# Kernel optimization log

Measured on AMD Instinct MI355X. Metric: run time of the kernel, lower is better.

## Reference

```python
import jax, jax.numpy as jnp
import numpy as np

B, T, DQ, DV, UNITS = 32, 2048, 1024, 1024, 1024


def setup_inputs() -> dict:
    key = jax.random.key(0)
    ks = jax.random.split(key, 11)
    s_q = 1.0 / np.sqrt(DQ)
    s_v = 1.0 / np.sqrt(DV)
    s_u = 1.0 / np.sqrt(UNITS)
    return {
        "query": jax.random.normal(ks[0], (B, DQ), jnp.float32),
        "values": jax.random.normal(ks[1], (B, T, DV), jnp.float32),
        "prev_coverage": jax.random.uniform(ks[2], (B, T, 1), jnp.float32),
        "Wh": jax.random.normal(ks[3], (DQ, UNITS), jnp.float32) * s_q,
        "bh": jnp.zeros((UNITS,), jnp.float32),
        "Ws": jax.random.normal(ks[4], (DV, UNITS), jnp.float32) * s_v,
        "bs": jnp.zeros((UNITS,), jnp.float32),
        "Wc": jax.random.normal(ks[5], (1, UNITS), jnp.float32),
        "bc": jnp.zeros((UNITS,), jnp.float32),
        "Vw": jax.random.normal(ks[6], (UNITS, 1), jnp.float32) * s_u,
        "Vb": jnp.zeros((1,), jnp.float32),
    }


def reference(query, values, prev_coverage, Wh, bh, Ws, bs, Wc, bc, Vw, Vb):
    # query: [B, DQ] -> [B, 1, UNITS] (broadcast over time)
    q_proj = (query @ Wh + bh)[:, None, :]
    # values: [B, T, DV] -> [B, T, UNITS]
    v_proj = jnp.einsum('btd,du->btu', values, Ws) + bs
    # prev_coverage: [B, T, 1] -> [B, T, UNITS]
    c_proj = prev_coverage * Wc[0] + bc
    # score: [B, T, 1] via inline MLP
    score = jnp.tanh(q_proj + v_proj + c_proj) @ Vw + Vb
    # softmax over time axis (axis=1)
    attention_weights = jax.nn.softmax(score, axis=1)  # [B, T, 1]
    coverage = attention_weights + prev_coverage       # [B, T, 1]
    context_vector = jnp.sum(attention_weights * values, axis=1)  # [B, DV]
    return context_vector, jnp.squeeze(attention_weights, -1), coverage
```

## Files before the change

kernel.cpp:

```cpp
#include <hip/hip_runtime.h>
#include <hip/hip_bf16.h>
#include <stdint.h>

#define NB 32
#define NT 2048
#define ND 1024
#define NU 1024

typedef __attribute__((ext_vector_type(8))) short bf16x8;
typedef __attribute__((ext_vector_type(4))) float f32x4;
typedef __attribute__((ext_vector_type(4))) unsigned short us4;

__device__ __forceinline__ unsigned short f2bf(float f) {
  unsigned int u = __float_as_uint(f);
  u = (u + 0x7fffu + ((u >> 16) & 1u)) >> 16;
  return (unsigned short)u;
}

__device__ __forceinline__ float tanh_fast(float x) {
  x = fminf(10.0f, fmaxf(-10.0f, x));
  float t = __expf(2.0f * x);
  return 1.0f - 2.0f * __builtin_amdgcn_rcpf(t + 1.0f);
}

__global__ void wst_kernel(const float* __restrict__ Ws,
                           unsigned short* __restrict__ Wst) {
  __shared__ float tile[32][33];
  int d0 = blockIdx.x * 32, u0 = blockIdx.y * 32;
  int c = threadIdx.x & 31, r8 = threadIdx.x >> 5;
#pragma unroll
  for (int i = 0; i < 4; ++i) {
    int rr = i * 8 + r8;
    tile[rr][c] = Ws[(size_t)(d0 + rr) * NU + u0 + c];
  }
  __syncthreads();
#pragma unroll
  for (int i = 0; i < 4; ++i) {
    int rr = i * 8 + r8;
    Wst[(size_t)(u0 + rr) * ND + d0 + c] = f2bf(tile[c][rr]);
  }
}

__global__ void qb_kernel(const float* __restrict__ query,
                          const float* __restrict__ Wh,
                          const float* __restrict__ bh,
                          const float* __restrict__ bs,
                          const float* __restrict__ bc,
                          float* __restrict__ qb) {
  int b = blockIdx.x, tid = threadIdx.x;
  int u = tid * 4;
  float ax = bh[u + 0] + bs[u + 0] + bc[u + 0];
  float ay = bh[u + 1] + bs[u + 1] + bc[u + 1];
  float az = bh[u + 2] + bs[u + 2] + bc[u + 2];
  float aw = bh[u + 3] + bs[u + 3] + bc[u + 3];
  const float* q = query + (size_t)b * ND;
  const float4* W4 = (const float4*)Wh;
  for (int d = 0; d < ND; ++d) {
    float qv = q[d];
    float4 w = W4[d * 256 + tid];
    ax = fmaf(qv, w.x, ax);
    ay = fmaf(qv, w.y, ay);
    az = fmaf(qv, w.z, az);
    aw = fmaf(qv, w.w, aw);
  }
  float4 o; o.x = ax; o.y = ay; o.z = az; o.w = aw;
  ((float4*)(qb + (size_t)b * NU))[tid] = o;
}

__launch_bounds__(256)
__global__ void score_gemm(const float* __restrict__ values,
                           const unsigned short* __restrict__ Wst,
                           const float* __restrict__ qb,
                           const float* __restrict__ cov,
                           const float* __restrict__ Wc,
                           const float* __restrict__ Vw,
                           float* __restrict__ scores) {
  const int uc = blockIdx.x;
  const int tc = blockIdx.y;
  const int b  = blockIdx.z;
  const int t0 = tc * 128, u0 = uc * 128;
  const int tid = threadIdx.x;

  __shared__ unsigned short As[128 * 40];
  __shared__ unsigned short Bs[128 * 40];
  __shared__ float covs[128], qbs[128], wcs[128], vws[128];

  if (tid < 128) {
    covs[tid] = cov[(size_t)b * NT + t0 + tid];
    qbs[tid]  = qb[(size_t)b * NU + u0 + tid];
    wcs[tid]  = Wc[u0 + tid];
    vws[tid]  = Vw[u0 + tid];
  }

  f32x4 acc[4][4];
#pragma unroll
  for (int i = 0; i < 4; ++i)
#pragma unroll
    for (int j = 0; j < 4; ++j)
      acc[i][j] = (f32x4){0.f, 0.f, 0.f, 0.f};

  const int lane = tid & 63;
  const int wave = tid >> 6;
  const int wm = wave >> 1, wn = wave & 1;
  const int q = lane >> 4, ln = lane & 15;

  const int ar = tid >> 3;
  const int ac = (tid & 7) * 4;
  const int brow = tid >> 2;
  const int bcol = (tid & 3) * 8;

  const float* Abase = values + (size_t)(b * NT + t0) * ND;
  const unsigned short* Bbase = Wst + (size_t)u0 * ND;

  for (int kk = 0; kk < ND; kk += 32) {
#pragma unroll
    for (int p = 0; p < 4; ++p) {
      int row = p * 32 + ar;
      float4 v = *(const float4*)(Abase + (size_t)row * ND + kk + ac);
      us4 h;
      h.x = f2bf(v.x); h.y = f2bf(v.y); h.z = f2bf(v.z); h.w = f2bf(v.w);
      *(us4*)&As[row * 40 + ac] = h;
    }
#pragma unroll
    for (int p = 0; p < 2; ++p) {
      int row = p * 64 + brow;
      uint4 v = *(const uint4*)(Bbase + (size_t)row * ND + kk + bcol);
      *(uint4*)&Bs[row * 40 + bcol] = v;
    }
    __syncthreads();

    bf16x8 a[4], bb[4];
#pragma unroll
    for (int i = 0; i < 4; ++i) {
      a[i]  = *(const bf16x8*)&As[(wm * 64 + i * 16 + ln) * 40 + q * 8];
      bb[i] = *(const bf16x8*)&Bs[(wn * 64 + i * 16 + ln) * 40 + q * 8];
    }
#pragma unroll
    for (int i = 0; i < 4; ++i)
#pragma unroll
      for (int j = 0; j < 4; ++j)
        acc[i][j] = __builtin_amdgcn_mfma_f32_16x16x32_bf16(a[i], bb[j], acc[i][j], 0, 0, 0);
    __syncthreads();
  }

  float part[4][4];
#pragma unroll
  for (int tm = 0; tm < 4; ++tm)
#pragma unroll
    for (int r = 0; r < 4; ++r) part[tm][r] = 0.f;

#pragma unroll
  for (int tn = 0; tn < 4; ++tn) {
    int n = wn * 64 + tn * 16 + ln;
    float qv = qbs[n], wc = wcs[n], vw = vws[n];
#pragma unroll
    for (int tm = 0; tm < 4; ++tm) {
#pragma unroll
      for (int r = 0; r < 4; ++r) {
        int m = wm * 64 + tm * 16 + q * 4 + r;
        float pre = acc[tm][tn][r] + qv + covs[m] * wc;
        part[tm][r] += vw * tanh_fast(pre);
      }
    }
  }
#pragma unroll
  for (int tm = 0; tm < 4; ++tm) {
#pragma unroll
    for (int r = 0; r < 4; ++r) {
      float v = part[tm][r];
      v += __shfl_xor(v, 1);
      v += __shfl_xor(v, 2);
      v += __shfl_xor(v, 4);
      v += __shfl_xor(v, 8);
      if (ln == 0) {
        int m = wm * 64 + tm * 16 + q * 4 + r;
        atomicAdd(&scores[(size_t)b * NT + t0 + m], v);
      }
    }
  }
}

__global__ void softmax_stats(const float* __restrict__ scores,
                              float* __restrict__ stats) {
  int b = blockIdx.x, tid = threadIdx.x;
  __shared__ float red[4], red2[4];
  const float* s = scores + (size_t)b * NT;
  float m = -1e30f;
  for (int t = tid; t < NT; t += 256) m = fmaxf(m, s[t]);
#pragma unroll
  for (int off = 1; off < 64; off <<= 1) m = fmaxf(m, __shfl_xor(m, off));
  if ((tid & 63) == 0) red[tid >> 6] = m;
  __syncthreads();
  m = fmaxf(fmaxf(red[0], red[1]), fmaxf(red[2], red[3]));
  float l = 0.f;
  for (int t = tid; t < NT; t += 256) l += __expf(s[t] - m);
#pragma unroll
  for (int off = 1; off < 64; off <<= 1) l += __shfl_xor(l, off);
  if ((tid & 63) == 0) red2[tid >> 6] = l;
  __syncthreads();
  if (tid == 0) {
    l = red2[0] + red2[1] + red2[2] + red2[3];
    stats[b] = m;
    stats[32 + b] = 1.0f / l;
  }
}

__global__ void weights_kernel(const float* __restrict__ scores,
                               const float* __restrict__ stats,
                               const float* __restrict__ cov,
                               float* __restrict__ out) {
  int idx = blockIdx.x * 256 + threadIdx.x;
  int b = idx >> 11;
  float w = __expf(scores[idx] - stats[b]) * stats[32 + b];
  out[32768 + idx] = w;
  out[32768 + 65536 + idx] = w + cov[idx];
}

__global__ void context_kernel(const float* __restrict__ values,
                               const float* __restrict__ attn,
                               float* __restrict__ ctx) {
  int b = blockIdx.y, t0 = blockIdx.x * 128, tid = threadIdx.x;
  const float4* v4 = (const float4*)(values + (size_t)b * NT * ND);
  const float* w = attn + (size_t)b * NT + t0;
  float ax = 0.f, ay = 0.f, az = 0.f, aw = 0.f;
  for (int t = 0; t < 128; ++t) {
    float wt = w[t];
    float4 x = v4[(size_t)(t0 + t) * 256 + tid];
    ax = fmaf(wt, x.x, ax);
    ay = fmaf(wt, x.y, ay);
    az = fmaf(wt, x.z, az);
    aw = fmaf(wt, x.w, aw);
  }
  float* c = ctx + (size_t)b * ND + tid * 4;
  atomicAdd(c + 0, ax);
  atomicAdd(c + 1, ay);
  atomicAdd(c + 2, az);
  atomicAdd(c + 3, aw);
}

extern "C" void kernel_launch(void* const* d_in, const int* in_sizes, int n_in,
                              void* d_out, int out_size, void* d_ws, size_t ws_size,
                              hipStream_t stream) {
  (void)in_sizes; (void)n_in; (void)out_size; (void)ws_size;
  const float* query  = (const float*)d_in[0];
  const float* values = (const float*)d_in[1];
  const float* cov    = (const float*)d_in[2];
  const float* Wh     = (const float*)d_in[3];
  const float* bh     = (const float*)d_in[4];
  const float* Ws     = (const float*)d_in[5];
  const float* bs     = (const float*)d_in[6];
  const float* Wc     = (const float*)d_in[7];
  const float* bc     = (const float*)d_in[8];
  const float* Vw     = (const float*)d_in[9];

  char* ws = (char*)d_ws;
  unsigned short* Wst = (unsigned short*)ws;
  float* qb     = (float*)(ws + 2u * 1024 * 1024);
  float* scores = (float*)(ws + 2u * 1024 * 1024 + 128u * 1024);
  float* stats  = (float*)(ws + 2u * 1024 * 1024 + 384u * 1024);

  float* out = (float*)d_out;

  hipMemsetAsync(scores, 0, (size_t)NB * NT * sizeof(float), stream);
  hipMemsetAsync(out, 0, (size_t)NB * ND * sizeof(float), stream);

  wst_kernel<<<dim3(32, 32), 256, 0, stream>>>(Ws, Wst);
  qb_kernel<<<NB, 256, 0, stream>>>(query, Wh, bh, bs, bc, qb);
  score_gemm<<<dim3(8, 16, 32), 256, 0, stream>>>(values, Wst, qb, cov, Wc, Vw, scores);
  softmax_stats<<<NB, 256, 0, stream>>>(scores, stats);
  weights_kernel<<<256, 256, 0, stream>>>(scores, stats, cov, out);
  context_kernel<<<dim3(16, 32), 256, 0, stream>>>(values, out + 32768, out);
}
```

Baseline: 741.9 us.

## Pre-convert values to bf16 and load GEMM tiles via global_load_lds

Adds a pass that converts the whole values tensor to bf16 in workspace, so the score GEMM loads half the bytes per tile and can use direct global-to-LDS loads with an XOR swizzle instead of register staging and in-loop conversion. The GEMM grid is remapped so blocks sharing a batch and time tile run adjacently, which should improve L2 reuse. The query projection is split across more blocks with a shared-memory reduction, and the softmax stats and weight kernels are fused into one. The conversion pass adds an extra full read of values plus a 128 MB write, and the path depends on the workspace being large enough, otherwise it falls back to the fp32 GEMM.

New measurement: 635.0 us. 1.17x faster.

```diff
diff --git a/kernel.cpp b/kernel.cpp
--- a/kernel.cpp
+++ b/kernel.cpp
@@ -10,6 +10,7 @@
 typedef __attribute__((ext_vector_type(8))) short bf16x8;
 typedef __attribute__((ext_vector_type(4))) float f32x4;
 typedef __attribute__((ext_vector_type(4))) unsigned short us4;
+typedef __attribute__((ext_vector_type(8))) unsigned short us8;
 
 __device__ __forceinline__ unsigned short f2bf(float f) {
   unsigned int u = __float_as_uint(f);
@@ -21,6 +22,23 @@
   x = fminf(10.0f, fmaxf(-10.0f, x));
   float t = __expf(2.0f * x);
   return 1.0f - 2.0f * __builtin_amdgcn_rcpf(t + 1.0f);
+}
+
+__device__ __forceinline__ void gload_lds16(const void* g, void* s) {
+  __builtin_amdgcn_global_load_lds(
+      (const __attribute__((address_space(1))) unsigned int*)g,
+      (__attribute__((address_space(3))) unsigned int*)s, 16, 0, 0);
+}
+
+__global__ void cvt_kernel(const float* __restrict__ v,
+                           unsigned short* __restrict__ o) {
+  size_t idx = ((size_t)blockIdx.x * 256 + threadIdx.x) * 8;
+  const float4* p = (const float4*)(v + idx);
+  float4 x = p[0], y = p[1];
+  us8 h;
+  h[0] = f2bf(x.x); h[1] = f2bf(x.y); h[2] = f2bf(x.z); h[3] = f2bf(x.w);
+  h[4] = f2bf(y.x); h[5] = f2bf(y.y); h[6] = f2bf(y.z); h[7] = f2bf(y.w);
+  *(us8*)(o + idx) = h;
 }
 
 __global__ void wst_kernel(const float* __restrict__ Ws,
@@ -41,48 +59,62 @@
   }
 }
 
-__global__ void qb_kernel(const float* __restrict__ query,
-                          const float* __restrict__ Wh,
-                          const float* __restrict__ bh,
-                          const float* __restrict__ bs,
-                          const float* __restrict__ bc,
-                          float* __restrict__ qb) {
-  int b = blockIdx.x, tid = threadIdx.x;
-  int u = tid * 4;
-  float ax = bh[u + 0] + bs[u + 0] + bc[u + 0];
-  float ay = bh[u + 1] + bs[u + 1] + bc[u + 1];
-  float az = bh[u + 2] + bs[u + 2] + bc[u + 2];
-  float aw = bh[u + 3] + bs[u + 3] + bc[u + 3];
-  const float* q = query + (size_t)b * ND;
-  const float4* W4 = (const float4*)Wh;
-  for (int d = 0; d < ND; ++d) {
+__global__ void qb_kernel2(const float* __restrict__ query,
+                           const float* __restrict__ Wh,
+                           const float* __restrict__ bh,
+                           const float* __restrict__ bs,
+                           const float* __restrict__ bc,
+                           float* __restrict__ qb) {
+  int uc = blockIdx.x, b = blockIdx.y;
+  int tid = threadIdx.x, ud = tid & 31, ds = tid >> 5;
+  const float* q = query + (size_t)b * ND + ds * 128;
+  const float4* W4 = (const float4*)Wh + (size_t)ds * 128 * 256 + uc * 32 + ud;
+  float4 a = {0.f, 0.f, 0.f, 0.f};
+  for (int d = 0; d < 128; ++d) {
     float qv = q[d];
-    float4 w = W4[d * 256 + tid];
-    ax = fmaf(qv, w.x, ax);
-    ay = fmaf(qv, w.y, ay);
-    az = fmaf(qv, w.z, az);
-    aw = fmaf(qv, w.w, aw);
-  }
-  float4 o; o.x = ax; o.y = ay; o.z = az; o.w = aw;
-  ((float4*)(qb + (size_t)b * NU))[tid] = o;
+    float4 w = W4[(size_t)d * 256];
+    a.x = fmaf(qv, w.x, a.x);
+    a.y = fmaf(qv, w.y, a.y);
+    a.z = fmaf(qv, w.z, a.z);
+    a.w = fmaf(qv, w.w, a.w);
+  }
+  __shared__ float4 red[8][32];
+  red[ds][ud] = a;
+  __syncthreads();
+  if (tid < 32) {
+    float4 s = red[0][tid];
+#pragma unroll
+    for (int r = 1; r < 8; ++r) {
+      float4 t = red[r][tid];
+      s.x += t.x; s.y += t.y; s.z += t.z; s.w += t.w;
+    }
+    int u = uc * 128 + tid * 4;
+    s.x += bh[u + 0] + bs[u + 0] + bc[u + 0];
+    s.y += bh[u + 1] + bs[u + 1] + bc[u + 1];
+    s.z += bh[u + 2] + bs[u + 2] + bc[u + 2];
+    s.w += bh[u + 3] + bs[u + 3] + bc[u + 3];
+    ((float4*)(qb + (size_t)b * NU))[uc * 32 + tid] = s;
+  }
 }
 
 __launch_bounds__(256)
-__global__ void score_gemm(const float* __restrict__ values,
-                           const unsigned short* __restrict__ Wst,
-                           const float* __restrict__ qb,
-                           const float* __restrict__ cov,
-                           const float* __restrict__ Wc,
-                           const float* __restrict__ Vw,
-                           float* __restrict__ scores) {
-  const int uc = blockIdx.x;
-  const int tc = blockIdx.y;
-  const int b  = blockIdx.z;
+__global__ void score_gemm_bf16(const unsigned short* __restrict__ vbf,
+                                const unsigned short* __restrict__ Wst,
+                                const float* __restrict__ qb,
+                                const float* __restrict__ cov,
+                                const float* __restrict__ Wc,
+                                const float* __restrict__ Vw,
+                                float* __restrict__ scores) {
+  int bid = blockIdx.x;
+  int g  = ((bid >> 6) << 3) | (bid & 7);
+  int uc = (bid >> 3) & 7;
+  int tc = g & 15;
+  int b  = g >> 4;
   const int t0 = tc * 128, u0 = uc * 128;
   const int tid = threadIdx.x;
 
-  __shared__ unsigned short As[128 * 40];
-  __shared__ unsigned short Bs[128 * 40];
+  __shared__ unsigned short As[128 * 32];
+  __shared__ unsigned short Bs[128 * 32];
   __shared__ float covs[128], qbs[128], wcs[128], vws[128];
 
   if (tid < 128) {
@@ -104,36 +136,34 @@
   const int wm = wave >> 1, wn = wave & 1;
   const int q = lane >> 4, ln = lane & 15;
 
-  const int ar = tid >> 3;
-  const int ac = (tid & 7) * 4;
-  const int brow = tid >> 2;
-  const int bcol = (tid & 3) * 8;
-
-  const float* Abase = values + (size_t)(b * NT + t0) * ND;
-  const unsigned short* Bbase = Wst + (size_t)u0 * ND;
+  const int Lr = lane >> 2;
+  const int cswz = (lane & 3) ^ ((Lr >> 1) & 3);
+  const unsigned short* pA0 = vbf + (size_t)(b * NT + t0 + wave * 32 + Lr) * ND + cswz * 8;
+  const unsigned short* pA1 = pA0 + (size_t)16 * ND;
+  const unsigned short* pB0 = Wst + (size_t)(u0 + wave * 32 + Lr) * ND + cswz * 8;
+  const unsigned short* pB1 = pB0 + (size_t)16 * ND;
+  unsigned short* sA0 = &As[(wave * 32) * 32];
+  unsigned short* sA1 = &As[(wave * 32 + 16) * 32];
+  unsigned short* sB0 = &Bs[(wave * 32) * 32];
+  unsigned short* sB1 = &Bs[(wave * 32 + 16) * 32];
+
+  const int swz8 = (q ^ ((ln >> 1) & 3)) * 8;
+  const unsigned short* aP = &As[(wm * 64 + ln) * 32 + swz8];
+  const unsigned short* bP = &Bs[(wn * 64 + ln) * 32 + swz8];
 
   for (int kk = 0; kk < ND; kk += 32) {
-#pragma unroll
-    for (int p = 0; p < 4; ++p) {
-      int row = p * 32 + ar;
-      float4 v = *(const float4*)(Abase + (size_t)row * ND + kk + ac);
-      us4 h;
-      h.x = f2bf(v.x); h.y = f2bf(v.y); h.z = f2bf(v.z); h.w = f2bf(v.w);
-      *(us4*)&As[row * 40 + ac] = h;
-    }
-#pragma unroll
-    for (int p = 0; p < 2; ++p) {
-      int row = p * 64 + brow;
-      uint4 v = *(const uint4*)(Bbase + (size_t)row * ND + kk + bcol);
-      *(uint4*)&Bs[row * 40 + bcol] = v;
-    }
+    gload_lds16(pA0, sA0);
+    gload_lds16(pA1, sA1);
+    gload_lds16(pB0, sB0);
+    gload_lds16(pB1, sB1);
+    pA0 += 32; pA1 += 32; pB0 += 32; pB1 += 32;
     __syncthreads();
 
     bf16x8 a[4], bb[4];
 #pragma unroll
     for (int i = 0; i < 4; ++i) {
-      a[i]  = *(const bf16x8*)&As[(wm * 64 + i * 16 + ln) * 40 + q * 8];
-      bb[i] = *(const bf16x8*)&Bs[(wn * 64 + i * 16 + ln) * 40 + q * 8];
+      a[i]  = *(const bf16x8*)(aP + i * 16 * 32);
+      bb[i] = *(const bf16x8*)(bP + i * 16 * 32);
     }
 #pragma unroll
     for (int i = 0; i < 4; ++i)
@@ -180,8 +210,122 @@
   }
 }
 
-__global__ void softmax_stats(const float* __restrict__ scores,
-                              float* __restrict__ stats) {
+__launch_bounds__(256)
+__global__ void score_gemm_f32(const float* __restrict__ values,
+                               const unsigned short* __restrict__ Wst,
+                               const float* __restrict__ qb,
+                               const float* __restrict__ cov,
+                               const float* __restrict__ Wc,
+                               const float* __restrict__ Vw,
+                               float* __restrict__ scores) {
+  const int uc = blockIdx.x;
+  const int tc = blockIdx.y;
+  const int b  = blockIdx.z;
+  const int t0 = tc * 128, u0 = uc * 128;
+  const int tid = threadIdx.x;
+
+  __shared__ unsigned short As[128 * 40];
+  __shared__ unsigned short Bs[128 * 40];
+  __shared__ float covs[128], qbs[128], wcs[128], vws[128];
+
+  if (tid < 128) {
+    covs[tid] = cov[(size_t)b * NT + t0 + tid];
+    qbs[tid]  = qb[(size_t)b * NU + u0 + tid];
+    wcs[tid]  = Wc[u0 + tid];
+    vws[tid]  = Vw[u0 + tid];
+  }
+
+  f32x4 acc[4][4];
+#pragma unroll
+  for (int i = 0; i < 4; ++i)
+#pragma unroll
+    for (int j = 0; j < 4; ++j)
+      acc[i][j] = (f32x4){0.f, 0.f, 0.f, 0.f};
+
+  const int lane = tid & 63;
+  const int wave = tid >> 6;
+  const int wm = wave >> 1, wn = wave & 1;
+  const int q = lane >> 4, ln = lane & 15;
+
+  const int ar = tid >> 3;
+  const int ac = (tid & 7) * 4;
+  const int brow = tid >> 2;
+  const int bcol = (tid & 3) * 8;
+
+  const float* Abase = values + (size_t)(b * NT + t0) * ND;
+  const unsigned short* Bbase = Wst + (size_t)u0 * ND;
+
+  for (int kk = 0; kk < ND; kk += 32) {
+#pragma unroll
+    for (int p = 0; p < 4; ++p) {
+      int row = p * 32 + ar;
+      float4 v = *(const float4*)(Abase + (size_t)row * ND + kk + ac);
+      us4 h;
+      h.x = f2bf(v.x); h.y = f2bf(v.y); h.z = f2bf(v.z); h.w = f2bf(v.w);
+      *(us4*)&As[row * 40 + ac] = h;
+    }
+#pragma unroll
+    for (int p = 0; p < 2; ++p) {
+      int row = p * 64 + brow;
+      uint4 v = *(const uint4*)(Bbase + (size_t)row * ND + kk + bcol);
+      *(uint4*)&Bs[row * 40 + bcol] = v;
+    }
+    __syncthreads();
+
+    bf16x8 a[4], bb[4];
+#pragma unroll
+    for (int i = 0; i < 4; ++i) {
+      a[i]  = *(const bf16x8*)&As[(wm * 64 + i * 16 + ln) * 40 + q * 8];
+      bb[i] = *(const bf16x8*)&Bs[(wn * 64 + i * 16 + ln) * 40 + q * 8];
+    }
+#pragma unroll
+    for (int i = 0; i < 4; ++i)
+#pragma unroll
+      for (int j = 0; j < 4; ++j)
+        acc[i][j] = __builtin_amdgcn_mfma_f32_16x16x32_bf16(a[i], bb[j], acc[i][j], 0, 0, 0);
+    __syncthreads();
+  }
+
+  float part[4][4];
+#pragma unroll
+  for (int tm = 0; tm < 4; ++tm)
+#pragma unroll
+    for (int r = 0; r < 4; ++r) part[tm][r] = 0.f;
+
+#pragma unroll
+  for (int tn = 0; tn < 4; ++tn) {
+    int n = wn * 64 + tn * 16 + ln;
+    float qv = qbs[n], wc = wcs[n], vw = vws[n];
+#pragma unroll
+    for (int tm = 0; tm < 4; ++tm) {
+#pragma unroll
+      for (int r = 0; r < 4; ++r) {
+        int m = wm * 64 + tm * 16 + q * 4 + r;
+        float pre = acc[tm][tn][r] + qv + covs[m] * wc;
+        part[tm][r] += vw * tanh_fast(pre);
+      }
+    }
+  }
+#pragma unroll
+  for (int tm = 0; tm < 4; ++tm) {
+#pragma unroll
+    for (int r = 0; r < 4; ++r) {
+      float v = part[tm][r];
+      v += __shfl_xor(v, 1);
+      v += __shfl_xor(v, 2);
+      v += __shfl_xor(v, 4);
+      v += __shfl_xor(v, 8);
+      if (ln == 0) {
+        int m = wm * 64 + tm * 16 + q * 4 + r;
+        atomicAdd(&scores[(size_t)b * NT + t0 + m], v);
+      }
+    }
+  }
+}
+
+__global__ void softmax_fused(const float* __restrict__ scores,
+                              const float* __restrict__ cov,
+                              float* __restrict__ out) {
   int b = blockIdx.x, tid = threadIdx.x;
   __shared__ float red[4], red2[4];
   const float* s = scores + (size_t)b * NT;
@@ -198,22 +342,13 @@
   for (int off = 1; off < 64; off <<= 1) l += __shfl_xor(l, off);
   if ((tid & 63) == 0) red2[tid >> 6] = l;
   __syncthreads();
-  if (tid == 0) {
-    l = red2[0] + red2[1] + red2[2] + red2[3];
-    stats[b] = m;
-    stats[32 + b] = 1.0f / l;
-  }
-}
-
-__global__ void weights_kernel(const float* __restrict__ scores,
-                               const float* __restrict__ stats,
-                               const float* __restrict__ cov,
-                               float* __restrict__ out) {
-  int idx = blockIdx.x * 256 + threadIdx.x;
-  int b = idx >> 11;
-  float w = __expf(scores[idx] - stats[b]) * stats[32 + b];
-  out[32768 + idx] = w;
-  out[32768 + 65536 + idx] = w + cov[idx];
+  float rl = 1.0f / (red2[0] + red2[1] + red2[2] + red2[3]);
+  for (int t = tid; t < NT; t += 256) {
+    float w = __expf(s[t] - m) * rl;
+    size_t idx = (size_t)b * NT + t;
+    out[32768 + idx] = w;
+    out[98304 + idx] = w + cov[idx];
+  }
 }
 
 __global__ void context_kernel(const float* __restrict__ values,
@@ -241,7 +376,7 @@
 extern "C" void kernel_launch(void* const* d_in, const int* in_sizes, int n_in,
                               void* d_out, int out_size, void* d_ws, size_t ws_size,
                               hipStream_t stream) {
-  (void)in_sizes; (void)n_in; (void)out_size; (void)ws_size;
+  (void)in_sizes; (void)n_in; (void)out_size;
   const float* query  = (const float*)d_in[0];
   const float* values = (const float*)d_in[1];
   const float* cov    = (const float*)d_in[2];
@@ -253,21 +388,39 @@
   const float* bc     = (const float*)d_in[8];
   const float* Vw     = (const float*)d_in[9];
 
+  float* out = (float*)d_out;
+
+  const size_t VBF_BYTES = (size_t)NB * NT * ND * 2;
+  const size_t need = VBF_BYTES + 2u * 1024 * 1024 + 128u * 1024 + 256u * 1024;
   char* ws = (char*)d_ws;
-  unsigned short* Wst = (unsigned short*)ws;
-  float* qb     = (float*)(ws + 2u * 1024 * 1024);
-  float* scores = (float*)(ws + 2u * 1024 * 1024 + 128u * 1024);
-  float* stats  = (float*)(ws + 2u * 1024 * 1024 + 384u * 1024);
-
-  float* out = (float*)d_out;
-
-  hipMemsetAsync(scores, 0, (size_t)NB * NT * sizeof(float), stream);
-  hipMemsetAsync(out, 0, (size_t)NB * ND * sizeof(float), stream);
-
-  wst_kernel<<<dim3(32, 32), 256, 0, stream>>>(Ws, Wst);
-  qb_kernel<<<NB, 256, 0, stream>>>(query, Wh, bh, bs, bc, qb);
-  score_gemm<<<dim3(8, 16, 32), 256, 0, stream>>>(values, Wst, qb, cov, Wc, Vw, scores);
-  softmax_stats<<<NB, 256, 0, stream>>>(scores, stats);
-  weights_kernel<<<256, 256, 0, stream>>>(scores, stats, cov, out);
-  context_kernel<<<dim3(16, 32), 256, 0, stream>>>(values, out + 32768, out);
-}
+
+  if (ws_size >= need) {
+    unsigned short* vbf = (unsigned short*)ws;
+    unsigned short* Wst = (unsigned short*)(ws + VBF_BYTES);
+    float* qb     = (float*)(ws + VBF_BYTES + 2u * 1024 * 1024);
+    float* scores = (float*)(ws + VBF_BYTES + 2u * 1024 * 1024 + 128u * 1024);
+
+    hipMemsetAsync(scores, 0, (size_t)NB * NT * sizeof(float), stream);
+    hipMemsetAsync(out, 0, (size_t)NB * ND * sizeof(float), stream);
+
+    cvt_kernel<<<32768, 256, 0, stream>>>(values, vbf);
+    wst_kernel<<<dim3(32, 32), 256, 0, stream>>>(Ws, Wst);
+    qb_kernel2<<<dim3(8, 32), 256, 0, stream>>>(query, Wh, bh, bs, bc, qb);
+    score_gemm_bf16<<<4096, 256, 0, stream>>>(vbf, Wst, qb, cov, Wc, Vw, scores);
+    softmax_fused<<<NB, 256, 0, stream>>>(scores, cov, out);
+    context_kernel<<<dim3(16, 32), 256, 0, stream>>>(values, out + 32768, out);
+  } else {
+    unsigned short* Wst = (unsigned short*)ws;
+    float* qb     = (float*)(ws + 2u * 1024 * 1024);
+    float* scores = (float*)(ws + 2u * 1024 * 1024 + 128u * 1024);
+
+    hipMemsetAsync(scores, 0, (size_t)NB * NT * sizeof(float), stream);
+    hipMemsetAsync(out, 0, (size_t)NB * ND * sizeof(float), stream);
+
+    wst_kernel<<<dim3(32, 32), 256, 0, stream>>>(Ws, Wst);
+    qb_kernel2<<<dim3(8, 32), 256, 0, stream>>>(query, Wh, bh, bs, bc, qb);
+    score_gemm_f32<<<dim3(8, 16, 32), 256, 0, stream>>>(values, Wst, qb, cov, Wc, Vw, scores);
+    softmax_fused<<<NB, 256, 0, stream>>>(scores, cov, out);
+    context_kernel<<<dim3(16, 32), 256, 0, stream>>>(values, out + 32768, out);
+  }
+}
```
